# Optimization experiments

Hardware: AMD Instinct MI355X
Metric: run time of the kernel (lower is better)

## Reference

```python
import jax, jax.numpy as jnp
import numpy as np

DIM = 1024
N_HEADS = 16
D_HEAD = DIM // N_HEADS


def setup_inputs() -> dict:
    key = jax.random.key(0)
    ks = jax.random.split(key, 7)
    s = DIM ** -0.5
    return {
        "x": jax.random.normal(ks[0], (4, 2048, DIM), dtype=jnp.float32),
        "Wq": jax.random.normal(ks[1], (DIM, DIM), dtype=jnp.float32) * s,
        "bq": jax.random.normal(ks[2], (DIM,), dtype=jnp.float32) * 0.02,
        "Wk": jax.random.normal(ks[3], (DIM, DIM), dtype=jnp.float32) * s,
        "bk": jax.random.normal(ks[4], (DIM,), dtype=jnp.float32) * 0.02,
        "Wv": jax.random.normal(ks[5], (DIM, DIM), dtype=jnp.float32) * s,
        "bv": jax.random.normal(ks[6], (DIM,), dtype=jnp.float32) * 0.02,
    }


def reference(x, Wq, bq, Wk, bk, Wv, bv):
    B, N, D = x.shape
    H, Dh = N_HEADS, D_HEAD

    def split_heads(t):
        # b n (h d) -> b h n d
        return t.reshape(B, N, H, Dh).transpose(0, 2, 1, 3)

    q = split_heads(x @ Wq + bq)
    k = split_heads(x @ Wk + bk)
    v = split_heads(x @ Wv + bv)

    scale = Dh ** -0.5
    logit = jnp.einsum("bhnd,bhmd->bhnm", q, k) * scale  # [B,H,N,N]
    attn = jax.nn.softmax(logit, axis=-1)
    out = jnp.einsum("bhnm,bhmd->bhnd", attn, v)
    # b h n d -> b n (h d)
    return out.transpose(0, 2, 1, 3).reshape(B, N, D)
```

## Files before the change

kernel.cpp:

```cpp
#include <hip/hip_runtime.h>
#include <hip/hip_bf16.h>
#include <stdint.h>

#define BB 4
#define SEQ 2048
#define DIM 1024
#define NH 16
#define DH 64
#define MM (BB*SEQ)

typedef unsigned short u16;
typedef __attribute__((ext_vector_type(8))) __bf16 bf16x8;
typedef __attribute__((ext_vector_type(4))) float floatx4;
typedef __attribute__((ext_vector_type(4))) unsigned short u16x4;

#define QSCALE 0.18033688011112042f

__device__ __forceinline__ u16 f2bf(float f) {
    union { float f; unsigned u; } v; v.f = f;
    unsigned u = v.u;
    u += 0x7FFF + ((u >> 16) & 1);
    return (u16)(u >> 16);
}

__device__ __forceinline__ bf16x8 ldb8(const u16* p) {
    return *(const bf16x8*)(const void*)p;
}

__device__ __forceinline__ void async_copy16(const u16* g, u16* l) {
    __builtin_amdgcn_global_load_lds(
        (const __attribute__((address_space(1))) unsigned int*)g,
        (__attribute__((address_space(3))) unsigned int*)l, 16, 0, 0);
}

__global__ __launch_bounds__(256)
void prep(const float* __restrict__ x, u16* __restrict__ xb,
          const float* __restrict__ Wq, const float* __restrict__ Wk,
          const float* __restrict__ Wv, u16* __restrict__ Wt) {
    const int bx = blockIdx.x;
    const int tid = threadIdx.x;
    if (bx < 8192) {
        const size_t i = ((size_t)bx * 256 + tid) * 4;
        float4 f = *(const float4*)(x + i);
        u16x4 o = { f2bf(f.x), f2bf(f.y), f2bf(f.z), f2bf(f.w) };
        *(u16x4*)(xb + i) = o;
        return;
    }
    const int idx = bx - 8192;
    const int t = idx >> 8;
    const int r2 = idx & 255;
    const int k0 = (r2 >> 4) * 64, n0 = (r2 & 15) * 64;
    const float* W = (t == 0) ? Wq : (t == 1) ? Wk : Wv;
    u16* D = Wt + (size_t)t * DIM * DIM;
    __shared__ u16 T[64][65];
    #pragma unroll
    for (int p = 0; p < 4; p++) {
        const int r = p * 16 + (tid >> 4), c = (tid & 15) * 4;
        float4 f = *(const float4*)(W + (size_t)(k0 + r) * DIM + n0 + c);
        T[c + 0][r] = f2bf(f.x); T[c + 1][r] = f2bf(f.y);
        T[c + 2][r] = f2bf(f.z); T[c + 3][r] = f2bf(f.w);
    }
    __syncthreads();
    #pragma unroll
    for (int p = 0; p < 4; p++) {
        const int rn = p * 16 + (tid >> 4), ck = (tid & 15) * 4;
        u16x4 v = { T[rn][ck], T[rn][ck + 1], T[rn][ck + 2], T[rn][ck + 3] };
        *(u16x4*)(D + (size_t)(n0 + rn) * DIM + k0 + ck) = v;
    }
}

__global__ __launch_bounds__(256, 3)
void qkv_gemm3(const u16* __restrict__ xb, const u16* __restrict__ Wt,
               const float* __restrict__ bq, const float* __restrict__ bk,
               const float* __restrict__ bv, u16* __restrict__ ws) {
    __shared__ u16 As[2][4096];
    __shared__ u16 Bs[2][4096];

    const int m0 = blockIdx.x * 128;
    const int t  = blockIdx.y >> 3;
    const int c0 = (blockIdx.y & 7) * 128;
    const u16* Wtb = Wt + (size_t)t * DIM * DIM;
    const float* bias = (t == 0) ? bq : (t == 1) ? bk : bv;
    const float osc = (t == 0) ? QSCALE : 1.0f;
    u16* dst = ws + (size_t)t * ((size_t)MM * DIM);

    const int tid  = threadIdx.x;
    const int lane = tid & 63;
    const int w    = tid >> 6;
    const int wr = w >> 1, wc = w & 1;
    const int g = lane >> 4, ln = lane & 15;

    floatx4 acc[4][4];
    #pragma unroll
    for (int i = 0; i < 4; i++)
        #pragma unroll
        for (int j = 0; j < 4; j++) acc[i][j] = (floatx4){0.f,0.f,0.f,0.f};

    const int srow = w*16 + (lane >> 2);
    const int gseg = (lane & 3) ^ ((lane >> 3) & 3);
    const u16* gA = xb  + (size_t)(m0 + srow) * DIM + gseg*8;
    const u16* gB = Wtb + (size_t)(c0 + srow) * DIM + gseg*8;

    async_copy16(gA,                   &As[0][w*512]);
    async_copy16(gA + (size_t)64*DIM,  &As[0][2048 + w*512]);
    async_copy16(gB,                   &Bs[0][w*512]);
    async_copy16(gB + (size_t)64*DIM,  &Bs[0][2048 + w*512]);
    __syncthreads();

    const int xu = (ln >> 1) & 3;

    for (int it = 0; it < 32; it++) {
        const int cur = it & 1;
        if (it < 31) {
            const int nxt = cur ^ 1;
            const int kk = (it + 1) * 32;
            async_copy16(gA + kk,                  &As[nxt][w*512]);
            async_copy16(gA + kk + (size_t)64*DIM, &As[nxt][2048 + w*512]);
            async_copy16(gB + kk,                  &Bs[nxt][w*512]);
            async_copy16(gB + kk + (size_t)64*DIM, &Bs[nxt][2048 + w*512]);
        }

        bf16x8 a[4], b[4];
        #pragma unroll
        for (int fr = 0; fr < 4; fr++)
            a[fr] = ldb8(&As[cur][(wr*64 + fr*16 + ln)*32 + (g ^ xu)*8]);
        #pragma unroll
        for (int fc = 0; fc < 4; fc++)
            b[fc] = ldb8(&Bs[cur][(wc*64 + fc*16 + ln)*32 + (g ^ xu)*8]);

        if (t < 2) {
            #pragma unroll
            for (int fr = 0; fr < 4; fr++)
                #pragma unroll
                for (int fc = 0; fc < 4; fc++)
                    acc[fr][fc] = __builtin_amdgcn_mfma_f32_16x16x32_bf16(
                        b[fc], a[fr], acc[fr][fc], 0, 0, 0);
        } else {
            #pragma unroll
            for (int fr = 0; fr < 4; fr++)
                #pragma unroll
                for (int fc = 0; fc < 4; fc++)
                    acc[fr][fc] = __builtin_amdgcn_mfma_f32_16x16x32_bf16(
                        a[fr], b[fc], acc[fr][fc], 0, 0, 0);
        }
        __syncthreads();
    }

    if (t < 2) {
        #pragma unroll
        for (int fc = 0; fc < 4; fc++) {
            const int cc = c0 + wc*64 + fc*16 + g*4;
            const float4 b4 = *(const float4*)&bias[cc];
            const int h = cc >> 6, d = cc & 63;
            #pragma unroll
            for (int fr = 0; fr < 4; fr++) {
                const int tok = m0 + wr*64 + fr*16 + ln;
                const int bidx = tok >> 11, nn = tok & 2047;
                u16x4 v = { f2bf((acc[fr][fc][0] + b4.x) * osc),
                            f2bf((acc[fr][fc][1] + b4.y) * osc),
                            f2bf((acc[fr][fc][2] + b4.z) * osc),
                            f2bf((acc[fr][fc][3] + b4.w) * osc) };
                *(u16x4*)&dst[((size_t)(bidx*NH + h)*SEQ + nn)*DH + d] = v;
            }
        }
    } else {
        #pragma unroll
        for (int fc = 0; fc < 4; fc++) {
            const int cc = c0 + wc*64 + fc*16 + ln;
            const float bias_v = bias[cc];
            const int h = cc >> 6, d = cc & 63;
            #pragma unroll
            for (int fr = 0; fr < 4; fr++) {
                const int mrow = m0 + wr*64 + fr*16 + g*4;
                const int bidx = mrow >> 11, nn = mrow & 2047;
                u16x4 v = { f2bf(acc[fr][fc][0] + bias_v), f2bf(acc[fr][fc][1] + bias_v),
                            f2bf(acc[fr][fc][2] + bias_v), f2bf(acc[fr][fc][3] + bias_v) };
                *(u16x4*)&dst[((size_t)(bidx*NH + h)*DH + d)*SEQ + nn] = v;
            }
        }
    }
}

#define LDA 40
__global__ __launch_bounds__(256)
void qkv_gemm(const float* __restrict__ x,
              const float* __restrict__ Wq, const float* __restrict__ bq,
              const float* __restrict__ Wk, const float* __restrict__ bk,
              const float* __restrict__ Wv, const float* __restrict__ bv,
              u16* __restrict__ ws) {
    __shared__ u16 As[128 * LDA];
    __shared__ u16 Bs[128 * LDA];
    const int m0 = blockIdx.x * 128;
    const int t  = blockIdx.y >> 3;
    const int c0 = (blockIdx.y & 7) * 128;
    const float* W    = (t == 0) ? Wq : (t == 1) ? Wk : Wv;
    const float* bias = (t == 0) ? bq : (t == 1) ? bk : bv;
    const float osc = (t == 0) ? QSCALE : 1.0f;
    u16* dst = ws + (size_t)t * ((size_t)MM * DIM);
    const int tid  = threadIdx.x;
    const int lane = tid & 63;
    const int wave = tid >> 6;
    const int wr = wave >> 1, wc = wave & 1;
    const int g = lane >> 4, ln = lane & 15;
    floatx4 acc[4][4];
    #pragma unroll
    for (int i = 0; i < 4; i++)
        #pragma unroll
        for (int j = 0; j < 4; j++) acc[i][j] = (floatx4){0.f,0.f,0.f,0.f};
    const int ar  = tid >> 1;
    const int ak  = (tid & 1) * 16;
    const int bkr = tid & 31;
    const int bc  = (tid >> 5) * 16;
    for (int kk = 0; kk < DIM; kk += 32) {
        {
            const float4* s4 = (const float4*)(x + (size_t)(m0 + ar) * DIM + kk + ak);
            float4 f0 = s4[0], f1 = s4[1], f2 = s4[2], f3 = s4[3];
            unsigned pk[8];
            pk[0] = f2bf(f0.x) | ((unsigned)f2bf(f0.y) << 16);
            pk[1] = f2bf(f0.z) | ((unsigned)f2bf(f0.w) << 16);
            pk[2] = f2bf(f1.x) | ((unsigned)f2bf(f1.y) << 16);
            pk[3] = f2bf(f1.z) | ((unsigned)f2bf(f1.w) << 16);
            pk[4] = f2bf(f2.x) | ((unsigned)f2bf(f2.y) << 16);
            pk[5] = f2bf(f2.z) | ((unsigned)f2bf(f2.w) << 16);
            pk[6] = f2bf(f3.x) | ((unsigned)f2bf(f3.y) << 16);
            pk[7] = f2bf(f3.z) | ((unsigned)f2bf(f3.w) << 16);
            uint4* d = (uint4*)&As[ar * LDA + ak];
            d[0] = make_uint4(pk[0], pk[1], pk[2], pk[3]);
            d[1] = make_uint4(pk[4], pk[5], pk[6], pk[7]);
        }
        {
            const float4* s4 = (const float4*)(W + (size_t)(kk + bkr) * DIM + c0 + bc);
            float4 f0 = s4[0], f1 = s4[1], f2 = s4[2], f3 = s4[3];
            float fv[16] = {f0.x,f0.y,f0.z,f0.w, f1.x,f1.y,f1.z,f1.w,
                            f2.x,f2.y,f2.z,f2.w, f3.x,f3.y,f3.z,f3.w};
            #pragma unroll
            for (int j = 0; j < 16; j++)
                Bs[(bc + j) * LDA + bkr] = f2bf(fv[j]);
        }
        __syncthreads();
        bf16x8 a[4], b[4];
        #pragma unroll
        for (int fr = 0; fr < 4; fr++)
            a[fr] = ldb8(&As[(wr*64 + fr*16 + ln) * LDA + g*8]);
        #pragma unroll
        for (int fc = 0; fc < 4; fc++)
            b[fc] = ldb8(&Bs[(wc*64 + fc*16 + ln) * LDA + g*8]);
        #pragma unroll
        for (int fr = 0; fr < 4; fr++)
            #pragma unroll
            for (int fc = 0; fc < 4; fc++)
                acc[fr][fc] = __builtin_amdgcn_mfma_f32_16x16x32_bf16(
                    a[fr], b[fc], acc[fr][fc], 0, 0, 0);
        __syncthreads();
    }
    #pragma unroll
    for (int fc = 0; fc < 4; fc++) {
        const int cc = c0 + wc*64 + fc*16 + ln;
        const float bias_v = bias[cc];
        const int h = cc >> 6, d = cc & 63;
        #pragma unroll
        for (int fr = 0; fr < 4; fr++) {
            #pragma unroll
            for (int rr = 0; rr < 4; rr++) {
                const int mrow = m0 + wr*64 + fr*16 + g*4 + rr;
                const int bidx = mrow >> 11, nn = mrow & 2047;
                const float val = (acc[fr][fc][rr] + bias_v) * osc;
                size_t idx;
                if (t < 2) idx = ((size_t)(bidx*NH + h)*SEQ + nn)*DH + d;
                else       idx = ((size_t)(bidx*NH + h)*DH + d)*SEQ + nn;
                dst[idx] = f2bf(val);
            }
        }
    }
}

#define LDP 72

__global__ __launch_bounds__(256, 2)
void attn5(const u16* __restrict__ ws, float* __restrict__ out) {
    const int qt = blockIdx.x;
    const int h  = blockIdx.y;
    const int b  = blockIdx.z;
    const int bh = b*NH + h;

    const u16* Qw = ws;
    const u16* Kw = ws + (size_t)MM * DIM;
    const u16* Vt = ws + 2 * (size_t)MM * DIM;

    __shared__ u16 Kbuf[2][4096];
    __shared__ u16 Vbuf[2][4096];
    __shared__ u16 P[4][64 * LDP];

    const int tid  = threadIdx.x;
    const int lane = tid & 63;
    const int w    = tid >> 6;
    const int g = lane >> 4, ln = lane & 15;
    const int q0 = qt*256 + w*64;

    const int srow = w*8 + (lane >> 3);
    const int sseg = (lane & 7) ^ ((lane >> 3) & 7);
    const u16* kg = Kw + ((size_t)bh*SEQ + srow)*DH + sseg*8;
    const u16* vg = Vt + ((size_t)bh*DH + srow)*SEQ + sseg*8;

    const int fs0 = ((0*4 + g) ^ (ln & 7)) * 8;
    const int fs1 = ((1*4 + g) ^ (ln & 7)) * 8;

    bf16x8 aq[4][2];
    #pragma unroll
    for (int rb = 0; rb < 4; rb++) {
        const u16* qp = Qw + ((size_t)bh*SEQ + q0 + rb*16 + ln)*DH + g*8;
        aq[rb][0] = ldb8(qp);
        aq[rb][1] = ldb8(qp + 32);
    }

    floatx4 acc[4][4];
    #pragma unroll
    for (int rb = 0; rb < 4; rb++)
        #pragma unroll
        for (int i = 0; i < 4; i++) acc[rb][i] = (floatx4){0.f,0.f,0.f,0.f};
    float lrun[4] = {0.f, 0.f, 0.f, 0.f};

    u16* Pw = &P[w][0];

    async_copy16(kg,                  &Kbuf[0][w*512]);
    async_copy16(kg + (size_t)32*DH,  &Kbuf[0][2048 + w*512]);
    async_copy16(vg,                  &Vbuf[0][w*512]);
    async_copy16(vg + (size_t)32*SEQ, &Vbuf[0][2048 + w*512]);
    __syncthreads();

    for (int kt = 0; kt < 32; kt++) {
        const int cur = kt & 1;
        if (kt < 31) {
            const int nxt = cur ^ 1;
            const size_t ko = (size_t)(kt + 1) * 64 * DH;
            const size_t vo = (size_t)(kt + 1) * 64;
            async_copy16(kg + ko,                  &Kbuf[nxt][w*512]);
            async_copy16(kg + ko + (size_t)32*DH,  &Kbuf[nxt][2048 + w*512]);
            async_copy16(vg + vo,                  &Vbuf[nxt][w*512]);
            async_copy16(vg + vo + (size_t)32*SEQ, &Vbuf[nxt][2048 + w*512]);
        }

        const u16* Kc = &Kbuf[cur][0];
        const u16* Vc = &Vbuf[cur][0];

        bf16x8 bkf[4][2];
        #pragma unroll
        for (int fn = 0; fn < 4; fn++) {
            bkf[fn][0] = ldb8(&Kc[(fn*16 + ln)*64 + fs0]);
            bkf[fn][1] = ldb8(&Kc[(fn*16 + ln)*64 + fs1]);
        }

        #pragma unroll
        for (int rb = 0; rb < 4; rb++) {
            #pragma unroll
            for (int fn = 0; fn < 4; fn++) {
                floatx4 z = (floatx4){0.f,0.f,0.f,0.f};
                z = __builtin_amdgcn_mfma_f32_16x16x32_bf16(bkf[fn][0], aq[rb][0], z, 0, 0, 0);
                z = __builtin_amdgcn_mfma_f32_16x16x32_bf16(bkf[fn][1], aq[rb][1], z, 0, 0, 0);
                float p0 = __builtin_amdgcn_exp2f(z[0]);
                float p1 = __builtin_amdgcn_exp2f(z[1]);
                float p2 = __builtin_amdgcn_exp2f(z[2]);
                float p3 = __builtin_amdgcn_exp2f(z[3]);
                lrun[rb] += (p0 + p1) + (p2 + p3);
                __hip_bfloat162 lo = __float22bfloat162_rn(make_float2(p0, p1));
                __hip_bfloat162 hi = __float22bfloat162_rn(make_float2(p2, p3));
                union { __hip_bfloat162 v2[2]; u16x4 v4; } u;
                u.v2[0] = lo; u.v2[1] = hi;
                *(u16x4*)&Pw[(rb*16 + ln)*LDP + fn*16 + g*4] = u.v4;
            }
        }

        bf16x8 av[4][2];
        #pragma unroll
        for (int fd = 0; fd < 4; fd++) {
            av[fd][0] = ldb8(&Vc[(fd*16 + ln)*64 + fs0]);
            av[fd][1] = ldb8(&Vc[(fd*16 + ln)*64 + fs1]);
        }
        bf16x8 bp[4][2];
        #pragma unroll
        for (int rb = 0; rb < 4; rb++) {
            bp[rb][0] = ldb8(&Pw[(rb*16 + ln)*LDP + g*8]);
            bp[rb][1] = ldb8(&Pw[(rb*16 + ln)*LDP + 32 + g*8]);
        }

        #pragma unroll
        for (int fd = 0; fd < 4; fd++)
            #pragma unroll
            for (int rb = 0; rb < 4; rb++) {
                acc[rb][fd] = __builtin_amdgcn_mfma_f32_16x16x32_bf16(av[fd][0], bp[rb][0], acc[rb][fd], 0, 0, 0);
                acc[rb][fd] = __builtin_amdgcn_mfma_f32_16x16x32_bf16(av[fd][1], bp[rb][1], acc[rb][fd], 0, 0, 0);
            }

        __syncthreads();
    }

    #pragma unroll
    for (int rb = 0; rb < 4; rb++) {
        float v = lrun[rb];
        v += __shfl_xor(v, 16, 64);
        v += __shfl_xor(v, 32, 64);
        lrun[rb] = v;
    }
    #pragma unroll
    for (int rb = 0; rb < 4; rb++) {
        const float inv = 1.0f / lrun[rb];
        const int n = q0 + rb*16 + ln;
        #pragma unroll
        for (int fd = 0; fd < 4; fd++) {
            floatx4 v = acc[rb][fd];
            float4 o = { v[0]*inv, v[1]*inv, v[2]*inv, v[3]*inv };
            *(float4*)&out[((size_t)b*SEQ + n)*DIM + h*DH + fd*16 + g*4] = o;
        }
    }
}

extern "C" void kernel_launch(void* const* d_in, const int* in_sizes, int n_in,
                              void* d_out, int out_size, void* d_ws, size_t ws_size,
                              hipStream_t stream) {
    const float* x  = (const float*)d_in[0];
    const float* Wq = (const float*)d_in[1];
    const float* bq = (const float*)d_in[2];
    const float* Wk = (const float*)d_in[3];
    const float* bk = (const float*)d_in[4];
    const float* Wv = (const float*)d_in[5];
    const float* bv = (const float*)d_in[6];
    u16* ws = (u16*)d_ws;
    float* out = (float*)d_out;

    const size_t need = (size_t)4 * MM * DIM * 2 + (size_t)3 * DIM * DIM * 2;
    if (ws_size >= need) {
        u16* xb = ws + (size_t)3 * MM * DIM;
        u16* Wt = ws + (size_t)4 * MM * DIM;
        prep<<<dim3(8192 + 768), 256, 0, stream>>>(x, xb, Wq, Wk, Wv, Wt);
        qkv_gemm3<<<dim3(MM/128, 24), 256, 0, stream>>>(xb, Wt, bq, bk, bv, ws);
    } else {
        qkv_gemm<<<dim3(MM/128, 24), 256, 0, stream>>>(x, Wq, bq, Wk, bk, Wv, bv, ws);
    }
    attn5<<<dim3(SEQ/256, NH, BB), 256, 0, stream>>>(ws, out);
}
```

Before: 259.1 us.

## Keep attention probabilities in registers and halve query tile per block

The attention kernel stops writing the bf16 probability tile to shared memory and reading it back. Because the QK^T accumulator layout matches the B-operand layout of the 16x16x16 bf16 MFMA, the exp'd scores feed the PV matmul straight from registers, with V fragments read using a matching swizzled offset. Each wave now handles 32 query rows instead of 64, which doubles the grid and lets four blocks share a CU. The trade-off is that each K/V tile is loaded twice as often across blocks, and the narrower k=16 MFMA issues more instructions for the PV product.

```diff
diff --git a/kernel.cpp b/kernel.cpp
--- a/kernel.cpp
+++ b/kernel.cpp
@@ -13,6 +13,7 @@
 typedef __attribute__((ext_vector_type(8))) __bf16 bf16x8;
 typedef __attribute__((ext_vector_type(4))) float floatx4;
 typedef __attribute__((ext_vector_type(4))) unsigned short u16x4;
+typedef __attribute__((ext_vector_type(4))) short short4v;
 
 #define QSCALE 0.18033688011112042f
 
@@ -31,6 +32,10 @@
     __builtin_amdgcn_global_load_lds(
         (const __attribute__((address_space(1))) unsigned int*)g,
         (__attribute__((address_space(3))) unsigned int*)l, 16, 0, 0);
+}
+
+__device__ __forceinline__ floatx4 mfma16(short4v a, short4v b, floatx4 c) {
+    return __builtin_amdgcn_mfma_f32_16x16x16bf16_1k(a, b, c, 0, 0, 0);
 }
 
 __global__ __launch_bounds__(256)
@@ -274,10 +279,8 @@
     }
 }
 
-#define LDP 72
-
-__global__ __launch_bounds__(256, 2)
-void attn5(const u16* __restrict__ ws, float* __restrict__ out) {
+__global__ __launch_bounds__(256, 4)
+void attn6(const u16* __restrict__ ws, float* __restrict__ out) {
     const int qt = blockIdx.x;
     const int h  = blockIdx.y;
     const int b  = blockIdx.z;
@@ -289,13 +292,12 @@
 
     __shared__ u16 Kbuf[2][4096];
     __shared__ u16 Vbuf[2][4096];
-    __shared__ u16 P[4][64 * LDP];
 
     const int tid  = threadIdx.x;
     const int lane = tid & 63;
     const int w    = tid >> 6;
     const int g = lane >> 4, ln = lane & 15;
-    const int q0 = qt*256 + w*64;
+    const int q0 = qt*128 + w*32;
 
     const int srow = w*8 + (lane >> 3);
     const int sseg = (lane & 7) ^ ((lane >> 3) & 7);
@@ -304,23 +306,24 @@
 
     const int fs0 = ((0*4 + g) ^ (ln & 7)) * 8;
     const int fs1 = ((1*4 + g) ^ (ln & 7)) * 8;
-
-    bf16x8 aq[4][2];
-    #pragma unroll
-    for (int rb = 0; rb < 4; rb++) {
+    const int vxor = ln & 7;
+    const int gh = g >> 1;
+    const int vh = (g & 1) * 4;
+
+    bf16x8 aq[2][2];
+    #pragma unroll
+    for (int rb = 0; rb < 2; rb++) {
         const u16* qp = Qw + ((size_t)bh*SEQ + q0 + rb*16 + ln)*DH + g*8;
         aq[rb][0] = ldb8(qp);
         aq[rb][1] = ldb8(qp + 32);
     }
 
-    floatx4 acc[4][4];
-    #pragma unroll
-    for (int rb = 0; rb < 4; rb++)
+    floatx4 acc[2][4];
+    #pragma unroll
+    for (int rb = 0; rb < 2; rb++)
         #pragma unroll
         for (int i = 0; i < 4; i++) acc[rb][i] = (floatx4){0.f,0.f,0.f,0.f};
-    float lrun[4] = {0.f, 0.f, 0.f, 0.f};
-
-    u16* Pw = &P[w][0];
+    float lrun[2] = {0.f, 0.f};
 
     async_copy16(kg,                  &Kbuf[0][w*512]);
     async_copy16(kg + (size_t)32*DH,  &Kbuf[0][2048 + w*512]);
@@ -343,72 +346,48 @@
         const u16* Kc = &Kbuf[cur][0];
         const u16* Vc = &Vbuf[cur][0];
 
-        bf16x8 bkf[4][2];
         #pragma unroll
         for (int fn = 0; fn < 4; fn++) {
-            bkf[fn][0] = ldb8(&Kc[(fn*16 + ln)*64 + fs0]);
-            bkf[fn][1] = ldb8(&Kc[(fn*16 + ln)*64 + fs1]);
-        }
-
-        #pragma unroll
-        for (int rb = 0; rb < 4; rb++) {
-            #pragma unroll
-            for (int fn = 0; fn < 4; fn++) {
+            bf16x8 k0 = ldb8(&Kc[(fn*16 + ln)*64 + fs0]);
+            bf16x8 k1 = ldb8(&Kc[(fn*16 + ln)*64 + fs1]);
+            short4v bp[2];
+            #pragma unroll
+            for (int rb = 0; rb < 2; rb++) {
                 floatx4 z = (floatx4){0.f,0.f,0.f,0.f};
-                z = __builtin_amdgcn_mfma_f32_16x16x32_bf16(bkf[fn][0], aq[rb][0], z, 0, 0, 0);
-                z = __builtin_amdgcn_mfma_f32_16x16x32_bf16(bkf[fn][1], aq[rb][1], z, 0, 0, 0);
+                z = __builtin_amdgcn_mfma_f32_16x16x32_bf16(k0, aq[rb][0], z, 0, 0, 0);
+                z = __builtin_amdgcn_mfma_f32_16x16x32_bf16(k1, aq[rb][1], z, 0, 0, 0);
                 float p0 = __builtin_amdgcn_exp2f(z[0]);
                 float p1 = __builtin_amdgcn_exp2f(z[1]);
                 float p2 = __builtin_amdgcn_exp2f(z[2]);
                 float p3 = __builtin_amdgcn_exp2f(z[3]);
                 lrun[rb] += (p0 + p1) + (p2 + p3);
-                __hip_bfloat162 lo = __float22bfloat162_rn(make_float2(p0, p1));
-                __hip_bfloat162 hi = __float22bfloat162_rn(make_float2(p2, p3));
-                union { __hip_bfloat162 v2[2]; u16x4 v4; } u;
-                u.v2[0] = lo; u.v2[1] = hi;
-                *(u16x4*)&Pw[(rb*16 + ln)*LDP + fn*16 + g*4] = u.v4;
+                union { __hip_bfloat162 h2[2]; short4v s4; } pu;
+                pu.h2[0] = __float22bfloat162_rn(make_float2(p0, p1));
+                pu.h2[1] = __float22bfloat162_rn(make_float2(p2, p3));
+                bp[rb] = pu.s4;
             }
-        }
-
-        bf16x8 av[4][2];
-        #pragma unroll
-        for (int fd = 0; fd < 4; fd++) {
-            av[fd][0] = ldb8(&Vc[(fd*16 + ln)*64 + fs0]);
-            av[fd][1] = ldb8(&Vc[(fd*16 + ln)*64 + fs1]);
-        }
-        bf16x8 bp[4][2];
-        #pragma unroll
-        for (int rb = 0; rb < 4; rb++) {
-            bp[rb][0] = ldb8(&Pw[(rb*16 + ln)*LDP + g*8]);
-            bp[rb][1] = ldb8(&Pw[(rb*16 + ln)*LDP + 32 + g*8]);
-        }
-
-        #pragma unroll
-        for (int fd = 0; fd < 4; fd++)
-            #pragma unroll
-            for (int rb = 0; rb < 4; rb++) {
-                acc[rb][fd] = __builtin_amdgcn_mfma_f32_16x16x32_bf16(av[fd][0], bp[rb][0], acc[rb][fd], 0, 0, 0);
-                acc[rb][fd] = __builtin_amdgcn_mfma_f32_16x16x32_bf16(av[fd][1], bp[rb][1], acc[rb][fd], 0, 0, 0);
+            const int vu = ((fn*2 + gh) ^ vxor) * 8 + vh;
+            #pragma unroll
+            for (int fd = 0; fd < 4; fd++) {
+                short4v av = *(const short4v*)(const void*)&Vc[(fd*16 + ln)*64 + vu];
+                acc[0][fd] = mfma16(av, bp[0], acc[0][fd]);
+                acc[1][fd] = mfma16(av, bp[1], acc[1][fd]);
             }
-
+        }
         __syncthreads();
     }
 
     #pragma unroll
-    for (int rb = 0; rb < 4; rb++) {
+    for (int rb = 0; rb < 2; rb++) {
         float v = lrun[rb];
         v += __shfl_xor(v, 16, 64);
         v += __shfl_xor(v, 32, 64);
-        lrun[rb] = v;
-    }
-    #pragma unroll
-    for (int rb = 0; rb < 4; rb++) {
-        const float inv = 1.0f / lrun[rb];
+        const float inv = 1.0f / v;
         const int n = q0 + rb*16 + ln;
         #pragma unroll
         for (int fd = 0; fd < 4; fd++) {
-            floatx4 v = acc[rb][fd];
-            float4 o = { v[0]*inv, v[1]*inv, v[2]*inv, v[3]*inv };
+            floatx4 vv = acc[rb][fd];
+            float4 o = { vv[0]*inv, vv[1]*inv, vv[2]*inv, vv[3]*inv };
             *(float4*)&out[((size_t)b*SEQ + n)*DIM + h*DH + fd*16 + g*4] = o;
         }
     }
@@ -436,5 +415,5 @@
     } else {
         qkv_gemm<<<dim3(MM/128, 24), 256, 0, stream>>>(x, Wq, bq, Wk, bk, Wv, bv, ws);
     }
-    attn5<<<dim3(SEQ/256, NH, BB), 256, 0, stream>>>(ws, out);
-}
+    attn6<<<dim3(SEQ/128, NH, BB), 256, 0, stream>>>(ws, out);
+}
```

Result: slower. 269.6 us (+4.1%).
